# Kernel tuning notes

Measured on AMD Instinct MI355X. Metric: run time of the kernel, lower is better.

## Reference

```python
import jax, jax.numpy as jnp
import numpy as np


def _diag_perm(h, w):
    # Matches torch loop: offsets -(h-1)..w-1, within offset ordered by row i.
    ii, jj = np.meshgrid(np.arange(h), np.arange(w), indexing='ij')
    idx = np.lexsort((ii.ravel(), (jj - ii).ravel())).astype(np.int32)
    inv = np.argsort(idx).astype(np.int32)
    return jnp.asarray(idx), jnp.asarray(inv)


def _mamba(tok, ln_g, ln_b, Win, conv_w, conv_b, Wx, Wdt, bdt, A_log, Dp, Wout):
    # tok: (B, L, C). MambaLayer = LayerNorm + standard Mamba block.
    di, dc = conv_w.shape
    ds = A_log.shape[-1]
    dtr = Wdt.shape[-1]
    mu = tok.mean(-1, keepdims=True)
    var = ((tok - mu) ** 2).mean(-1, keepdims=True)
    t = (tok - mu) * jax.lax.rsqrt(var + 1e-5) * ln_g + ln_b
    xz = jnp.einsum('blc,ec->ble', t, Win)          # (B,L,2*di)
    xh, z = jnp.split(xz, 2, axis=-1)
    # causal depthwise conv over sequence
    xc = jnp.transpose(xh, (0, 2, 1))               # (B,di,L)
    xc = jax.lax.conv_general_dilated(
        xc, conv_w[:, None, :], (1,), [(dc - 1, 0)],
        dimension_numbers=('NCH', 'OIH', 'NCH'), feature_group_count=di)
    u = jax.nn.silu(jnp.transpose(xc, (0, 2, 1)) + conv_b)  # (B,L,di)
    proj = jnp.einsum('bld,ed->ble', u, Wx)
    dt_r, Bm, Cm = jnp.split(proj, [dtr, dtr + ds], axis=-1)
    dt = jax.nn.softplus(jnp.einsum('blr,dr->bld', dt_r, Wdt) + bdt)  # (B,L,di)
    A = -jnp.exp(A_log)                              # (di,ds)

    def step(h, inp):
        dt_t, B_t, C_t, u_t = inp                    # (B,di) (B,ds) (B,ds) (B,di)
        dA = jnp.exp(dt_t[..., None] * A)            # (B,di,ds)
        h = dA * h + dt_t[..., None] * B_t[:, None, :] * u_t[..., None]
        y = jnp.einsum('bds,bs->bd', h, C_t)
        return h, y

    h0 = jnp.zeros((u.shape[0], di, ds), u.dtype)
    _, ys = jax.lax.scan(step, h0, (jnp.moveaxis(dt, 1, 0), jnp.moveaxis(Bm, 1, 0),
                                    jnp.moveaxis(Cm, 1, 0), jnp.moveaxis(u, 1, 0)))
    y = jnp.moveaxis(ys, 0, 1) + u * Dp              # (B,L,di)
    y = y * jax.nn.silu(z)
    return jnp.einsum('bld,cd->blc', y, Wout)


def _forward(x, ln_g, ln_b, Win, conv_w, conv_b, Wx, Wdt, bdt, A_log, Dp, Wout):
    b, c, h, w = x.shape
    idx, inv = _diag_perm(h, w)

    def mam(d, tok):
        return _mamba(tok, ln_g[d], ln_b[d], Win[d], conv_w[d], conv_b[d],
                      Wx[d], Wdt[d], bdt[d], A_log[d], Dp[d], Wout[d])

    row_tok = x.reshape(b, c, h * w).transpose(0, 2, 1)
    row_feat = mam(0, row_tok).transpose(0, 2, 1).reshape(b, c, h, w)
    col_tok = x.transpose(0, 1, 3, 2).reshape(b, c, w * h).transpose(0, 2, 1)
    col_feat = mam(1, col_tok).transpose(0, 2, 1).reshape(b, c, w, h).transpose(0, 1, 3, 2)
    diag_feat = mam(2, row_tok[:, idx, :])[:, inv, :].transpose(0, 2, 1).reshape(b, c, h, w)
    xf = x[:, :, :, ::-1]
    anti_tok = xf.reshape(b, c, h * w).transpose(0, 2, 1)[:, idx, :]
    anti_feat = mam(3, anti_tok)[:, inv, :].transpose(0, 2, 1).reshape(b, c, h, w)[:, :, :, ::-1]
    gate = jax.nn.sigmoid((row_feat + col_feat + diag_feat + anti_feat) / 4.0)
    return x * gate


def setup_inputs() -> dict:
    key = jax.random.key(0)
    ks = jax.random.split(key, 8)
    B, C, H, W = 4, 96, 48, 48
    DI, DS, DC, DTR = 192, 16, 4, 6
    s = 0.05
    return {
        'x': jax.random.normal(ks[0], (B, C, H, W), jnp.float32),
        'ln_g': jnp.ones((4, C), jnp.float32),
        'ln_b': jnp.zeros((4, C), jnp.float32),
        'Win': jax.random.normal(ks[1], (4, 2 * DI, C), jnp.float32) * s,
        'conv_w': jax.random.normal(ks[2], (4, DI, DC), jnp.float32) * s,
        'conv_b': jnp.zeros((4, DI), jnp.float32),
        'Wx': jax.random.normal(ks[3], (4, DTR + 2 * DS, DI), jnp.float32) * s,
        'Wdt': jax.random.normal(ks[4], (4, DI, DTR), jnp.float32) * s,
        'bdt': jax.random.normal(ks[5], (4, DI), jnp.float32) * s,
        'A_log': jnp.log(jnp.broadcast_to(jnp.arange(1, DS + 1, dtype=jnp.float32), (4, DI, DS))),
        'Dp': jnp.ones((4, DI), jnp.float32),
        'Wout': jax.random.normal(ks[6], (4, C, DI), jnp.float32) * s,
    }


def reference(x, ln_g, ln_b, Win, conv_w, conv_b, Wx, Wdt, bdt, A_log, Dp, Wout):
    return _forward(x, ln_g, ln_b, Win, conv_w, conv_b, Wx, Wdt, bdt, A_log, Dp, Wout)
```

## Files before the change

kernel.cpp:

```cpp
#include <hip/hip_runtime.h>
#include <math.h>

#define LSEQ 2304
#define LC 32
#define NCH 72

typedef unsigned short u16;
typedef unsigned int u32;
typedef __attribute__((ext_vector_type(8))) short bf16x8;
typedef __attribute__((ext_vector_type(4))) float f32x4;

__device__ __forceinline__ float sigmoidf_(float v){ return 1.f/(1.f+__expf(-v)); }
__device__ __forceinline__ u16 f2b(float f){
  union{float f; u32 u;} v; v.f = f;
  u32 r = v.u + 0x7fffu + ((v.u >> 16) & 1u);
  return (u16)(r >> 16);
}
__device__ __forceinline__ float b2f(u16 h){
  union{u32 u; float f;} v; v.u = ((u32)h) << 16; return v.f;
}
__device__ __forceinline__ u16 f2h(float f){
  _Float16 h = (_Float16)f;
  union{_Float16 h; u16 u;} v; v.h = h; return v.u;
}
__device__ __forceinline__ float h2f(u16 u){
  union{u16 u; _Float16 h;} v; v.u = u; return (float)v.h;
}
__device__ __forceinline__ uint2 pack4(float a, float b, float c, float d){
  uint2 o;
  o.x = (u32)f2b(a) | ((u32)f2b(b) << 16);
  o.y = (u32)f2b(c) | ((u32)f2b(d) << 16);
  return o;
}
__device__ __forceinline__ float softplus_(float v){
  return fmaxf(v, 0.f) + __logf(1.f + __expf(-fabsf(v)));
}

__global__ void prep_fold(const float* __restrict__ Win, const float* __restrict__ ln_g,
                          const float* __restrict__ ln_b, const float* __restrict__ A_log,
                          const float* __restrict__ Wout, const float* __restrict__ Wx,
                          const float* __restrict__ Wdt, const float* __restrict__ bdt,
                          u16* __restrict__ WinMF, float* __restrict__ b2,
                          float* __restrict__ Aneg2, u16* __restrict__ WoutMF,
                          u16* __restrict__ Wcomb, float* __restrict__ bcomb,
                          int* __restrict__ g, int* __restrict__ flag){
  int i = blockIdx.x * 256 + threadIdx.x;
  if (i < LSEQ){
    int l = i;
    g[l] = l;
    g[LSEQ + l] = (l % 48) * 48 + l / 48;
    int p = i;
    int ii = p / 48, jj = p % 48, dd = jj - ii;
    int off = (dd <= 0) ? (47 + dd) * (48 + dd) / 2
                        : 1176 + 48 * (dd - 1) - dd * (dd - 1) / 2;
    int l2 = off + min(ii, jj);
    g[2 * LSEQ + l2] = p;
    g[3 * LSEQ + l2] = ii * 48 + 47 - jj;
  }
  if (i < 4*192*16){
    float a = -expf(A_log[i]);
    Aneg2[i] = a * 1.44269504f;
    int s = i & 15;
    float a0 = -expf(A_log[i - s]);
    if (fabsf(a - (float)(s + 1) * a0) > 1e-5f * fabsf(a) + 1e-30f)
      atomicOr(flag, 1);
  }
  if (i < 4*384*96){
    int d = i / 36864, r = i % 36864, c = r % 96;
    WinMF[i] = f2b(Win[i] * ln_g[d*96 + c]);
  }
  if (i < 4*96*192) WoutMF[i] = f2b(Wout[i]);
  if (i < 4*224*192){
    int d = i / 43008, r = i % 43008, e = r / 192, c = r % 192;
    float w;
    if (e < 192){
      const float* wdt = &Wdt[(size_t)(d*192 + e) * 6];
      w = 0.f;
      #pragma unroll
      for (int r6 = 0; r6 < 6; ++r6) w += wdt[r6] * Wx[(size_t)(d*38 + r6) * 192 + c];
    } else if (e < 208){
      w = Wx[(size_t)(d*38 + 6 + (e - 192)) * 192 + c];
    } else {
      w = Wx[(size_t)(d*38 + 22 + (e - 208)) * 192 + c];
    }
    Wcomb[i] = f2b(w);
  }
  if (i < 4*224){
    int d = i / 224, e = i % 224;
    bcomb[i] = (e < 192) ? bdt[d*192 + e] : 0.f;
  }
  if (i < 4*384){
    int d = i / 384;
    const float* wr = &Win[(size_t)i * 96];
    const float* lb = &ln_b[d * 96];
    float s = 0.f;
    for (int c = 0; c < 96; ++c) s += wr[c] * lb[c];
    b2[i] = s;
  }
}

__global__ __launch_bounds__(256) void ln_kernel(const float* __restrict__ x, u16* __restrict__ n){
  __shared__ float red[512];
  int tid = threadIdx.x;
  int s = tid & 63, q = tid >> 6;
  int T = blockIdx.x * 64 + s;
  int b = T / 2304, p = T % 2304;
  const float* xp = x + (size_t)b * 96 * 2304 + p;
  float vals[24];
  float sum = 0.f, ss = 0.f;
  #pragma unroll
  for (int k = 0; k < 24; ++k){
    float v = xp[(size_t)(q*24 + k) * 2304];
    vals[k] = v; sum += v; ss += v*v;
  }
  red[q*64 + s] = sum;
  red[256 + q*64 + s] = ss;
  __syncthreads();
  float S = red[s] + red[64+s] + red[128+s] + red[192+s];
  float Q = red[256+s] + red[320+s] + red[384+s] + red[448+s];
  float mu = S * (1.f/96.f);
  float var = Q * (1.f/96.f) - mu*mu;
  float rs = rsqrtf(var + 1e-5f);
  u32 w[12];
  #pragma unroll
  for (int k = 0; k < 12; ++k){
    float v0 = (vals[2*k]   - mu) * rs;
    float v1 = (vals[2*k+1] - mu) * rs;
    w[k] = (u32)f2b(v0) | ((u32)f2b(v1) << 16);
  }
  uint4* np_ = (uint4*)(n + (size_t)T * 96 + q*24);
  np_[0] = make_uint4(w[0], w[1], w[2],  w[3]);
  np_[1] = make_uint4(w[4], w[5], w[6],  w[7]);
  np_[2] = make_uint4(w[8], w[9], w[10], w[11]);
}

__global__ __launch_bounds__(256) void kproj(const u16* __restrict__ nbf,
    const u16* __restrict__ WinMF, const float* __restrict__ b2,
    u16* __restrict__ xz){
  int d = blockIdx.y;
  int wv = threadIdx.x >> 6, lane = threadIdx.x & 63;
  int lr = lane & 15, lg = lane >> 4;
  int r0 = blockIdx.x * 64 + wv * 16;
  const u16* Ap = nbf + (size_t)(r0 + lr) * 96 + lg * 8;
  bf16x8 tk0 = *(const bf16x8*)(Ap);
  bf16x8 tk1 = *(const bf16x8*)(Ap + 32);
  bf16x8 tk2 = *(const bf16x8*)(Ap + 64);
  const u16* Wb = WinMF + (size_t)d * 36864 + (size_t)lr * 96 + lg * 8;
  const float* b2d = b2 + d * 384;
  u16* out = xz + ((size_t)d * 9216 + r0 + lr) * 384;
  for (int grp = 0; grp < 3; ++grp){
    f32x4 acc[8];
    #pragma unroll
    for (int t = 0; t < 8; ++t)
      acc[t] = *(const f32x4*)&b2d[(grp*8 + t)*16 + lg*4];
    #pragma unroll
    for (int t = 0; t < 8; ++t){
      const u16* wp = Wb + (size_t)(grp*8 + t) * 1536;
      acc[t] = __builtin_amdgcn_mfma_f32_16x16x32_bf16(*(const bf16x8*)(wp     ), tk0, acc[t], 0, 0, 0);
      acc[t] = __builtin_amdgcn_mfma_f32_16x16x32_bf16(*(const bf16x8*)(wp + 32), tk1, acc[t], 0, 0, 0);
      acc[t] = __builtin_amdgcn_mfma_f32_16x16x32_bf16(*(const bf16x8*)(wp + 64), tk2, acc[t], 0, 0, 0);
    }
    #pragma unroll
    for (int t = 0; t < 8; ++t){
      uint2 o = pack4(acc[t][0], acc[t][1], acc[t][2], acc[t][3]);
      *(uint2*)&out[(grp*8 + t)*16 + lg*4] = o;
    }
  }
}

__global__ __launch_bounds__(256) void kconv(const u16* __restrict__ xz, const int* __restrict__ g,
    const float* __restrict__ conv_w, const float* __restrict__ conv_b,
    u16* __restrict__ u, u16* __restrict__ sz){
  __shared__ u16 xh[67][200];
  int d = blockIdx.z, b = blockIdx.y, l0 = blockIdx.x * 64;
  int tid = threadIdx.x;
  const int* gd = g + d * LSEQ;
  const u16* xzd = xz + (size_t)d * 9216 * 384 + (size_t)b * LSEQ * 384;
  for (int i = tid; i < 67*24; i += 256){
    int lt = i / 24, j = i % 24;
    int gl = l0 - 3 + lt;
    uint4 v = make_uint4(0u, 0u, 0u, 0u);
    if (gl >= 0){
      int p = gd[gl];
      v = *(const uint4*)(xzd + (size_t)p * 384 + j * 8);
    }
    *(uint4*)&xh[lt][j*8] = v;
  }
  size_t obase = ((size_t)(d*4 + b) * LSEQ + l0) * 192;
  for (int i = tid; i < 64*48; i += 256){
    int lt = i / 48, j = (i % 48) * 4;
    int p = gd[l0 + lt];
    uint2 zv = *(const uint2*)(xzd + (size_t)p * 384 + 192 + j);
    float z0 = b2f((u16)(zv.x & 0xffff)), z1 = b2f((u16)(zv.x >> 16));
    float z2 = b2f((u16)(zv.y & 0xffff)), z3 = b2f((u16)(zv.y >> 16));
    z0 *= sigmoidf_(z0); z1 *= sigmoidf_(z1); z2 *= sigmoidf_(z2); z3 *= sigmoidf_(z3);
    *(uint2*)(sz + obase + (size_t)lt * 192 + j) = pack4(z0, z1, z2, z3);
  }
  __syncthreads();
  for (int i = tid; i < 64*48; i += 256){
    int lt = i / 48, j = (i % 48) * 4;
    float a0 = conv_b[d*192 + j + 0];
    float a1 = conv_b[d*192 + j + 1];
    float a2 = conv_b[d*192 + j + 2];
    float a3 = conv_b[d*192 + j + 3];
    const float4 w0 = *(const float4*)&conv_w[(size_t)(d*192 + j + 0) * 4];
    const float4 w1 = *(const float4*)&conv_w[(size_t)(d*192 + j + 1) * 4];
    const float4 w2 = *(const float4*)&conv_w[(size_t)(d*192 + j + 2) * 4];
    const float4 w3 = *(const float4*)&conv_w[(size_t)(d*192 + j + 3) * 4];
    const float* w0p = (const float*)&w0;
    const float* w1p = (const float*)&w1;
    const float* w2p = (const float*)&w2;
    const float* w3p = (const float*)&w3;
    #pragma unroll
    for (int kk = 0; kk < 4; ++kk){
      uint2 xv = *(const uint2*)&xh[lt + kk][j];
      a0 += w0p[kk] * b2f((u16)(xv.x & 0xffff));
      a1 += w1p[kk] * b2f((u16)(xv.x >> 16));
      a2 += w2p[kk] * b2f((u16)(xv.y & 0xffff));
      a3 += w3p[kk] * b2f((u16)(xv.y >> 16));
    }
    a0 *= sigmoidf_(a0); a1 *= sigmoidf_(a1); a2 *= sigmoidf_(a2); a3 *= sigmoidf_(a3);
    *(uint2*)(u + obase + (size_t)lt * 192 + j) = pack4(a0, a1, a2, a3);
  }
}

__global__ __launch_bounds__(256) void kernBM(const u16* __restrict__ u,
    const u16* __restrict__ Wcomb, const float* __restrict__ bcomb,
    u16* __restrict__ dtb, float* __restrict__ Bm, float* __restrict__ Cm){
  __shared__ u16 ush[64 * 200];
  int d = blockIdx.y;
  int tid = threadIdx.x;
  int tile0 = blockIdx.x * 64;
  const u16* ub = u + ((size_t)d * 4 * LSEQ + tile0) * 192;
  for (int i = tid; i < 64*24; i += 256){
    int row = i / 24, c8 = i % 24;
    *(uint4*)&ush[row*200 + c8*8] = *(const uint4*)&ub[(size_t)row*192 + c8*8];
  }
  __syncthreads();
  int wv = tid >> 6, lane = tid & 63;
  int lr = lane & 15, lg = lane >> 4;
  const u16* urow = &ush[(wv*16 + lr)*200 + lg*8];
  bf16x8 tk[6];
  #pragma unroll
  for (int kc = 0; kc < 6; ++kc) tk[kc] = *(const bf16x8*)(urow + kc*32);
  const u16* Wb = Wcomb + (size_t)d * 224 * 192 + (size_t)lr * 192 + lg * 8;
  bf16x8 bw[2][6];
  #pragma unroll
  for (int kc = 0; kc < 6; ++kc) bw[0][kc] = *(const bf16x8*)(Wb + kc*32);
  size_t tokrow = (size_t)d * 4 * LSEQ + tile0 + wv*16 + lr;
  for (int t = 0; t < 14; ++t){
    int cur = t & 1;
    if (t < 13){
      const u16* wp = Wb + (size_t)(t + 1) * 3072;
      #pragma unroll
      for (int kc = 0; kc < 6; ++kc) bw[cur^1][kc] = *(const bf16x8*)(wp + kc*32);
    }
    f32x4 a = (f32x4){0.f, 0.f, 0.f, 0.f};
    #pragma unroll
    for (int kc = 0; kc < 6; ++kc)
      a = __builtin_amdgcn_mfma_f32_16x16x32_bf16(bw[cur][kc], tk[kc], a, 0, 0, 0);
    if (t < 12){
      f32x4 bb = *(const f32x4*)&bcomb[d*224 + t*16 + lg*4];
      float s0 = softplus_(a[0] + bb[0]);
      float s1 = softplus_(a[1] + bb[1]);
      float s2 = softplus_(a[2] + bb[2]);
      float s3 = softplus_(a[3] + bb[3]);
      uint2 o;
      o.x = (u32)f2h(s0) | ((u32)f2h(s1) << 16);
      o.y = (u32)f2h(s2) | ((u32)f2h(s3) << 16);
      *(uint2*)&dtb[tokrow * 192 + t*16 + lg*4] = o;
    } else if (t == 12){
      *(float4*)&Bm[tokrow * 16 + lg*4] = make_float4(a[0], a[1], a[2], a[3]);
    } else {
      *(float4*)&Cm[tokrow * 16 + lg*4] = make_float4(a[0], a[1], a[2], a[3]);
    }
  }
}

__global__ __launch_bounds__(192) void kernC1(const u16* __restrict__ dtb, const u16* __restrict__ u,
    const float* __restrict__ Bm, const float* __restrict__ Cm,
    const float* __restrict__ Aneg2, const int* __restrict__ flag,
    u16* __restrict__ hfin, float* __restrict__ Send, u32* __restrict__ yS){
  __shared__ float Bsh[LC*16];
  __shared__ float Csh[LC*16];
  __shared__ u16 dtsh[LC*192];
  __shared__ u16 ush2[LC*192];
  int ch = blockIdx.x, b = blockIdx.y, d = blockIdx.z;
  int seq = d*4 + b;
  int di = threadIdx.x;
  size_t tb = (size_t)seq * LSEQ + ch * LC;
  const float* bp = Bm + tb * 16;
  const float* cp = Cm + tb * 16;
  for (int i = di; i < LC*16; i += 192){ Bsh[i] = bp[i]; Csh[i] = cp[i]; }
  {
    const uint4* dt4 = (const uint4*)(dtb + tb * 192);
    const uint4* u4  = (const uint4*)(u   + tb * 192);
    #pragma unroll
    for (int i = di; i < 768; i += 192){
      *(uint4*)&dtsh[i*8] = dt4[i];
      *(uint4*)&ush2[i*8] = u4[i];
    }
  }
  u32* ySp = yS + tb * 192;
  float h[16];
  #pragma unroll
  for (int s = 0; s < 16; ++s) h[s] = 0.f;
  float Sacc = 0.f;
  __syncthreads();
  if (*flag == 0){
    float A2_0 = Aneg2[(d*192 + di) * 16];
    for (int j = 0; j < LC; ++j){
      float dtv = h2f(dtsh[j*192 + di]);
      float uv  = b2f(ush2[j*192 + di]);
      float Bs[16], Cs[16];
      {
        const float4* b4 = (const float4*)&Bsh[j * 16];
        const float4* c4 = (const float4*)&Csh[j * 16];
        #pragma unroll
        for (int q = 0; q < 4; ++q){
          float4 v = b4[q]; Bs[q*4]=v.x; Bs[q*4+1]=v.y; Bs[q*4+2]=v.z; Bs[q*4+3]=v.w;
          float4 w = c4[q]; Cs[q*4]=w.x; Cs[q*4+1]=w.y; Cs[q*4+2]=w.z; Cs[q*4+3]=w.w;
        }
      }
      float dtu = dtv * uv;
      float e1 = __builtin_amdgcn_exp2f(dtv * A2_0);
      float e2 = e1*e1, e4 = e2*e2, e8 = e4*e4;
      float p[8];
      p[0]=e1; p[1]=e2; p[2]=e1*e2; p[3]=e4; p[4]=e1*e4; p[5]=e2*e4; p[6]=p[2]*e4; p[7]=e8;
      float yv = 0.f;
      #pragma unroll
      for (int s = 0; s < 8; ++s){
        h[s] = p[s]*h[s] + dtu*Bs[s];
        yv += h[s]*Cs[s];
        float q = p[s]*e8;
        h[s+8] = q*h[s+8] + dtu*Bs[s+8];
        yv += h[s+8]*Cs[s+8];
      }
      Sacc += dtv;
      ySp[j*192 + di] = (u32)f2h(yv) | ((u32)f2h(Sacc) << 16);
    }
  } else {
    float A2[16];
    {
      const float4* ap = (const float4*)&Aneg2[(d*192 + di) * 16];
      #pragma unroll
      for (int q = 0; q < 4; ++q){ float4 a4 = ap[q]; A2[q*4]=a4.x; A2[q*4+1]=a4.y; A2[q*4+2]=a4.z; A2[q*4+3]=a4.w; }
    }
    for (int j = 0; j < LC; ++j){
      float dtv = h2f(dtsh[j*192 + di]);
      float uv  = b2f(ush2[j*192 + di]);
      float Bs[16], Cs[16];
      {
        const float4* b4 = (const float4*)&Bsh[j * 16];
        const float4* c4 = (const float4*)&Csh[j * 16];
        #pragma unroll
        for (int q = 0; q < 4; ++q){
          float4 v = b4[q]; Bs[q*4]=v.x; Bs[q*4+1]=v.y; Bs[q*4+2]=v.z; Bs[q*4+3]=v.w;
          float4 w = c4[q]; Cs[q*4]=w.x; Cs[q*4+1]=w.y; Cs[q*4+2]=w.z; Cs[q*4+3]=w.w;
        }
      }
      float dtu = dtv * uv;
      float yv = 0.f;
      #pragma unroll
      for (int s = 0; s < 16; ++s){
        h[s] = __builtin_amdgcn_exp2f(dtv * A2[s]) * h[s] + dtu * Bs[s];
        yv += h[s] * Cs[s];
      }
      Sacc += dtv;
      ySp[j*192 + di] = (u32)f2h(yv) | ((u32)f2h(Sacc) << 16);
    }
  }
  u16* hf = &hfin[((size_t)seq * NCH + ch) * 3072 + di * 16];
  uint4 o0, o1;
  o0.x = (u32)f2b(h[0])  | ((u32)f2b(h[1])  << 16);
  o0.y = (u32)f2b(h[2])  | ((u32)f2b(h[3])  << 16);
  o0.z = (u32)f2b(h[4])  | ((u32)f2b(h[5])  << 16);
  o0.w = (u32)f2b(h[6])  | ((u32)f2b(h[7])  << 16);
  o1.x = (u32)f2b(h[8])  | ((u32)f2b(h[9])  << 16);
  o1.y = (u32)f2b(h[10]) | ((u32)f2b(h[11]) << 16);
  o1.z = (u32)f2b(h[12]) | ((u32)f2b(h[13]) << 16);
  o1.w = (u32)f2b(h[14]) | ((u32)f2b(h[15]) << 16);
  *(uint4*)hf = o0;
  *(uint4*)(hf + 8) = o1;
  Send[((size_t)seq * NCH + ch) * 192 + di] = Sacc;
}

__global__ __launch_bounds__(256) void kernC2(const u16* __restrict__ hfin, const float* __restrict__ Send,
    const float* __restrict__ Aneg2, u16* __restrict__ hin){
  int t = blockIdx.x * 256 + threadIdx.x;
  int seq = t / 3072, q = t % 3072;
  int di = q >> 4, s = q & 15;
  int d = seq >> 2;
  float A2 = Aneg2[(d*192 + di)*16 + s];
  float hr = 0.f;
  const u16* hf = hfin + (size_t)seq * NCH * 3072 + q;
  u16* hi = hin + (size_t)seq * NCH * 3072 + q;
  const float* Se = Send + (size_t)seq * NCH * 192 + di;
  for (int ch = 0; ch < NCH; ch += 8){
    float Se8[8]; u16 hf8[8];
    #pragma unroll
    for (int k = 0; k < 8; ++k){
      Se8[k] = Se[(size_t)(ch+k) * 192];
      hf8[k] = hf[(size_t)(ch+k) * 3072];
    }
    #pragma unroll
    for (int k = 0; k < 8; ++k){
      hi[(size_t)(ch+k) * 3072] = f2b(hr);
      hr = b2f(hf8[k]) + __builtin_amdgcn_exp2f(A2 * Se8[k]) * hr;
    }
  }
}

__global__ __launch_bounds__(384) void kscan2out(const u32* __restrict__ yS, const u16* __restrict__ u,
    const float* __restrict__ Cm,
    const float* __restrict__ Aneg2, const int* __restrict__ flag, const u16* __restrict__ hin,
    const u16* __restrict__ sz, const float* __restrict__ Dp,
    const u16* __restrict__ WoutMF, const int* __restrict__ g,
    u16* __restrict__ feat){
  __shared__ float Csh[64*16];
  __shared__ u16 vsh[64][200];
  int b = blockIdx.y, d = blockIdx.z;
  int seq = d*4 + b;
  int l0 = blockIdx.x * 64;
  int tid = threadIdx.x;
  int gc = tid / 192, di = tid % 192;
  int ch = blockIdx.x * 2 + gc;
  {
    const float* cp = Cm + ((size_t)seq * LSEQ + l0) * 16;
    for (int i = tid; i < 64*16; i += 384) Csh[i] = cp[i];
  }
  float hs[16];
  {
    const uint4* hi4 = (const uint4*)&hin[((size_t)seq * NCH + ch) * 3072 + di * 16];
    uint4 v0 = hi4[0], v1 = hi4[1];
    hs[0]=b2f((u16)(v0.x&0xffff)); hs[1]=b2f((u16)(v0.x>>16));
    hs[2]=b2f((u16)(v0.y&0xffff)); hs[3]=b2f((u16)(v0.y>>16));
    hs[4]=b2f((u16)(v0.z&0xffff)); hs[5]=b2f((u16)(v0.z>>16));
    hs[6]=b2f((u16)(v0.w&0xffff)); hs[7]=b2f((u16)(v0.w>>16));
    hs[8]=b2f((u16)(v1.x&0xffff)); hs[9]=b2f((u16)(v1.x>>16));
    hs[10]=b2f((u16)(v1.y&0xffff)); hs[11]=b2f((u16)(v1.y>>16));
    hs[12]=b2f((u16)(v1.z&0xffff)); hs[13]=b2f((u16)(v1.z>>16));
    hs[14]=b2f((u16)(v1.w&0xffff)); hs[15]=b2f((u16)(v1.w>>16));
  }
  float Dpv = Dp[d*192 + di];
  size_t tb = (size_t)seq * LSEQ + ch * LC;
  const u32* ySp = yS + tb * 192;
  const u16* up  = u   + tb * 192;
  const u16* szp = sz  + tb * 192;
  __syncthreads();
  if (*flag == 0){
    float A2_0 = Aneg2[(d*192 + di) * 16];
    #pragma unroll
    for (int jb = 0; jb < 4; ++jb){
      u32 ys8[8]; u16 uu8[8], zz8[8];
      #pragma unroll
      for (int k = 0; k < 8; ++k){
        int j = jb*8 + k;
        ys8[k] = ySp[j*192 + di];
        uu8[k] = up[j*192 + di];
        zz8[k] = szp[j*192 + di];
      }
      #pragma unroll
      for (int k = 0; k < 8; ++k){
        int j = jb*8 + k;
        float yv = h2f((u16)(ys8[k] & 0xffff));
        float Sc = h2f((u16)(ys8[k] >> 16));
        float uv = b2f(uu8[k]);
        float Cs[16];
        {
          const float4* c4 = (const float4*)&Csh[(gc*32 + j) * 16];
          #pragma unroll
          for (int q = 0; q < 4; ++q){ float4 w = c4[q]; Cs[q*4]=w.x; Cs[q*4+1]=w.y; Cs[q*4+2]=w.z; Cs[q*4+3]=w.w; }
        }
        float e1 = __builtin_amdgcn_exp2f(Sc * A2_0);
        float e2 = e1*e1, e4 = e2*e2, e8 = e4*e4;
        float p[8];
        p[0]=e1; p[1]=e2; p[2]=e1*e2; p[3]=e4; p[4]=e1*e4; p[5]=e2*e4; p[6]=p[2]*e4; p[7]=e8;
        float corr = 0.f;
        #pragma unroll
        for (int s = 0; s < 8; ++s){
          corr += p[s]    * hs[s]   * Cs[s];
          corr += p[s]*e8 * hs[s+8] * Cs[s+8];
        }
        float szv = b2f(zz8[k]);
        vsh[gc*32 + j][di] = f2b((yv + corr + uv * Dpv) * szv);
      }
    }
  } else {
    float A2[16];
    {
      const float4* ap = (const float4*)&Aneg2[(d*192 + di) * 16];
      #pragma unroll
      for (int q = 0; q < 4; ++q){ float4 a4 = ap[q]; A2[q*4]=a4.x; A2[q*4+1]=a4.y; A2[q*4+2]=a4.z; A2[q*4+3]=a4.w; }
    }
    #pragma unroll
    for (int jb = 0; jb < 4; ++jb){
      u32 ys8[8]; u16 uu8[8], zz8[8];
      #pragma unroll
      for (int k = 0; k < 8; ++k){
        int j = jb*8 + k;
        ys8[k] = ySp[j*192 + di];
        uu8[k] = up[j*192 + di];
        zz8[k] = szp[j*192 + di];
      }
      #pragma unroll
      for (int k = 0; k < 8; ++k){
        int j = jb*8 + k;
        float yv = h2f((u16)(ys8[k] & 0xffff));
        float Sc = h2f((u16)(ys8[k] >> 16));
        float uv = b2f(uu8[k]);
        float Cs[16];
        {
          const float4* c4 = (const float4*)&Csh[(gc*32 + j) * 16];
          #pragma unroll
          for (int q = 0; q < 4; ++q){ float4 w = c4[q]; Cs[q*4]=w.x; Cs[q*4+1]=w.y; Cs[q*4+2]=w.z; Cs[q*4+3]=w.w; }
        }
        float corr = 0.f;
        #pragma unroll
        for (int s = 0; s < 16; ++s)
          corr += __builtin_amdgcn_exp2f(Sc * A2[s]) * hs[s] * Cs[s];
        float szv = b2f(zz8[k]);
        vsh[gc*32 + j][di] = f2b((yv + corr + uv * Dpv) * szv);
      }
    }
  }
  __syncthreads();
  if (tid < 256){
    int wv = tid >> 6, lane = tid & 63;
    int lr = lane & 15, lg = lane >> 4;
    bf16x8 tk[6];
    #pragma unroll
    for (int kc = 0; kc < 6; ++kc)
      tk[kc] = *(const bf16x8*)&vsh[wv*16 + lr][kc*32 + lg*8];
    const u16* Wb = WoutMF + (size_t)d * 18432 + (size_t)lr * 192 + lg * 8;
    f32x4 acc[6];
    #pragma unroll
    for (int t = 0; t < 6; ++t) acc[t] = (f32x4){0.f, 0.f, 0.f, 0.f};
    #pragma unroll
    for (int t = 0; t < 6; ++t){
      const u16* wp = Wb + (size_t)t * 3072;
      #pragma unroll
      for (int kc = 0; kc < 6; ++kc)
        acc[t] = __builtin_amdgcn_mfma_f32_16x16x32_bf16(*(const bf16x8*)(wp + kc*32), tk[kc], acc[t], 0, 0, 0);
    }
    u16* fd = feat + (size_t)seq * LSEQ * 96;
    int p = g[d*LSEQ + l0 + wv*16 + lr];
    #pragma unroll
    for (int t = 0; t < 6; ++t){
      uint2 o = pack4(acc[t][0], acc[t][1], acc[t][2], acc[t][3]);
      *(uint2*)&fd[(size_t)p * 96 + t*16 + lg*4] = o;
    }
  }
}

__global__ __launch_bounds__(256) void kernE(const float* __restrict__ x, const u16* __restrict__ feat,
    float* __restrict__ out){
  __shared__ float acc[64 * 97];
  int p0 = blockIdx.x * 64, b = blockIdx.y;
  int tid = threadIdx.x;
  const size_t DS_ = (size_t)4 * LSEQ * 96;
  size_t base = ((size_t)b * LSEQ + p0) * 96;
  for (int i = tid; i < 3072; i += 256){
    int pp = i / 48, c2 = (i % 48) * 2;
    size_t o = base + (size_t)pp * 96 + c2;
    u32 v0 = *(const u32*)(feat + o);
    u32 v1 = *(const u32*)(feat + DS_ + o);
    u32 v2 = *(const u32*)(feat + 2*DS_ + o);
    u32 v3 = *(const u32*)(feat + 3*DS_ + o);
    float s0 = b2f((u16)(v0 & 0xffff)) + b2f((u16)(v1 & 0xffff)) + b2f((u16)(v2 & 0xffff)) + b2f((u16)(v3 & 0xffff));
    float s1 = b2f((u16)(v0 >> 16)) + b2f((u16)(v1 >> 16)) + b2f((u16)(v2 >> 16)) + b2f((u16)(v3 >> 16));
    acc[pp*97 + c2] = s0;
    acc[pp*97 + c2 + 1] = s1;
  }
  __syncthreads();
  for (int i = tid; i < 6144; i += 256){
    int c = i / 64, pp = i % 64;
    size_t o = ((size_t)b * 96 + c) * LSEQ + p0 + pp;
    out[o] = x[o] * sigmoidf_(acc[pp*97 + c] * 0.25f);
  }
}

extern "C" void kernel_launch(void* const* d_in, const int* in_sizes, int n_in,
                              void* d_out, int out_size, void* d_ws, size_t ws_size,
                              hipStream_t stream) {
  const float* x      = (const float*)d_in[0];
  const float* ln_g   = (const float*)d_in[1];
  const float* ln_b   = (const float*)d_in[2];
  const float* Win    = (const float*)d_in[3];
  const float* conv_w = (const float*)d_in[4];
  const float* conv_b = (const float*)d_in[5];
  const float* Wx     = (const float*)d_in[6];
  const float* Wdt    = (const float*)d_in[7];
  const float* bdt    = (const float*)d_in[8];
  const float* A_log  = (const float*)d_in[9];
  const float* Dp     = (const float*)d_in[10];
  const float* Wout   = (const float*)d_in[11];

  char* W = (char*)d_ws;
  char* W0 = W;
  auto alloc = [&](size_t bytes) -> char* {
    char* p = W; W += (bytes + 255) & ~(size_t)255; return p;
  };
  int*   g      = (int*)  alloc((size_t)4 * LSEQ * 4);
  int*   flag   = (int*)  alloc(256);
  float* Aneg2  = (float*)alloc((size_t)4 * 192 * 16 * 4);
  float* b2     = (float*)alloc((size_t)4 * 384 * 4);
  u16*   WinMF  = (u16*)  alloc((size_t)4 * 384 * 96 * 2);
  u16*   WoutMF = (u16*)  alloc((size_t)4 * 96 * 192 * 2);
  u16*   Wcomb  = (u16*)  alloc((size_t)4 * 224 * 192 * 2);
  float* bcomb  = (float*)alloc((size_t)4 * 224 * 4);
  u16*   nbf    = (u16*)  alloc((size_t)9216 * 96 * 2);
  u16*   xz     = (u16*)  alloc((size_t)4 * 9216 * 384 * 2);
  u16*   ubf    = (u16*)  alloc((size_t)16 * LSEQ * 192 * 2);
  u16*   szbf   = (u16*)  alloc((size_t)16 * LSEQ * 192 * 2);
  u16*   dtb    = (u16*)  alloc((size_t)16 * LSEQ * 192 * 2);
  float* Bm     = (float*)alloc((size_t)16 * LSEQ * 16 * 4);
  float* Cm     = (float*)alloc((size_t)16 * LSEQ * 16 * 4);
  u32*   ySbuf  = (u32*)  alloc((size_t)16 * LSEQ * 192 * 4);
  float* Send   = (float*)alloc((size_t)16 * NCH * 192 * 4);
  u16*   hfin   = (u16*)  alloc((size_t)16 * NCH * 3072 * 2);
  u16*   hin    = (u16*)  alloc((size_t)16 * NCH * 3072 * 2);
  u16*   feat   = (u16*)  alloc((size_t)16 * LSEQ * 96 * 2);
  if ((size_t)(W - W0) > ws_size) return;

  hipMemsetAsync(flag, 0, sizeof(int), stream);
  prep_fold<<<768, 256, 0, stream>>>(Win, ln_g, ln_b, A_log, Wout, Wx, Wdt, bdt,
                                     WinMF, b2, Aneg2, WoutMF, Wcomb, bcomb, g, flag);
  ln_kernel<<<144, 256, 0, stream>>>(x, nbf);
  kproj<<<dim3(144, 4), 256, 0, stream>>>(nbf, WinMF, b2, xz);
  kconv<<<dim3(36, 4, 4), 256, 0, stream>>>(xz, g, conv_w, conv_b, ubf, szbf);
  kernBM<<<dim3(144, 4), 256, 0, stream>>>(ubf, Wcomb, bcomb, dtb, Bm, Cm);
  kernC1<<<dim3(NCH, 4, 4), 192, 0, stream>>>(dtb, ubf, Bm, Cm, Aneg2, flag, hfin, Send, ySbuf);
  kernC2<<<192, 256, 0, stream>>>(hfin, Send, Aneg2, hin);
  kscan2out<<<dim3(36, 4, 4), 384, 0, stream>>>(ySbuf, ubf, Cm, Aneg2, flag, hin, szbf, Dp,
                                                WoutMF, g, feat);
  kernE<<<dim3(36, 4), 256, 0, stream>>>(x, feat, (float*)d_out);
}
```

Measured before the change: 190.5 us.

## Fuse dt/B/C projection kernel into chunk-scan kernel via shared memory

Merges the MFMA projection that produces dt, B and C into the first chunked selective-scan kernel. Each 384-thread block projects a 64-token tile into shared memory and then runs two 32-token scan chunks from it. This removes the global dtb and Bm buffers and one kernel launch. The cost is that 128 threads sit idle during the projection phase, blocks are larger, more shared memory is used per block, and there are fewer blocks than the old scan grid.

```diff
diff --git a/kernel.cpp b/kernel.cpp
--- a/kernel.cpp
+++ b/kernel.cpp
@@ -224,98 +224,84 @@
   }
 }
 
-__global__ __launch_bounds__(256) void kernBM(const u16* __restrict__ u,
+__global__ __launch_bounds__(384) void kBMC1(const u16* __restrict__ u,
     const u16* __restrict__ Wcomb, const float* __restrict__ bcomb,
-    u16* __restrict__ dtb, float* __restrict__ Bm, float* __restrict__ Cm){
-  __shared__ u16 ush[64 * 200];
-  int d = blockIdx.y;
+    const float* __restrict__ Aneg2, const int* __restrict__ flag,
+    float* __restrict__ Cm, u32* __restrict__ yS,
+    u16* __restrict__ hfin, float* __restrict__ Send){
+  __shared__ u16 ush[64*200];
+  __shared__ u16 dtsh[64*200];
+  __shared__ float Bsh[64*20];
+  __shared__ float Csh[64*20];
+  int tile = blockIdx.x, b = blockIdx.y, d = blockIdx.z;
+  int seq = d*4 + b;
   int tid = threadIdx.x;
-  int tile0 = blockIdx.x * 64;
-  const u16* ub = u + ((size_t)d * 4 * LSEQ + tile0) * 192;
-  for (int i = tid; i < 64*24; i += 256){
+  size_t tokbase = (size_t)seq * LSEQ + tile * 64;
+  const u16* ub = u + tokbase * 192;
+  for (int i = tid; i < 64*24; i += 384){
     int row = i / 24, c8 = i % 24;
     *(uint4*)&ush[row*200 + c8*8] = *(const uint4*)&ub[(size_t)row*192 + c8*8];
   }
   __syncthreads();
-  int wv = tid >> 6, lane = tid & 63;
-  int lr = lane & 15, lg = lane >> 4;
-  const u16* urow = &ush[(wv*16 + lr)*200 + lg*8];
-  bf16x8 tk[6];
-  #pragma unroll
-  for (int kc = 0; kc < 6; ++kc) tk[kc] = *(const bf16x8*)(urow + kc*32);
-  const u16* Wb = Wcomb + (size_t)d * 224 * 192 + (size_t)lr * 192 + lg * 8;
-  bf16x8 bw[2][6];
-  #pragma unroll
-  for (int kc = 0; kc < 6; ++kc) bw[0][kc] = *(const bf16x8*)(Wb + kc*32);
-  size_t tokrow = (size_t)d * 4 * LSEQ + tile0 + wv*16 + lr;
-  for (int t = 0; t < 14; ++t){
-    int cur = t & 1;
-    if (t < 13){
-      const u16* wp = Wb + (size_t)(t + 1) * 3072;
-      #pragma unroll
-      for (int kc = 0; kc < 6; ++kc) bw[cur^1][kc] = *(const bf16x8*)(wp + kc*32);
-    }
-    f32x4 a = (f32x4){0.f, 0.f, 0.f, 0.f};
-    #pragma unroll
-    for (int kc = 0; kc < 6; ++kc)
-      a = __builtin_amdgcn_mfma_f32_16x16x32_bf16(bw[cur][kc], tk[kc], a, 0, 0, 0);
-    if (t < 12){
-      f32x4 bb = *(const f32x4*)&bcomb[d*224 + t*16 + lg*4];
-      float s0 = softplus_(a[0] + bb[0]);
-      float s1 = softplus_(a[1] + bb[1]);
-      float s2 = softplus_(a[2] + bb[2]);
-      float s3 = softplus_(a[3] + bb[3]);
-      uint2 o;
-      o.x = (u32)f2h(s0) | ((u32)f2h(s1) << 16);
-      o.y = (u32)f2h(s2) | ((u32)f2h(s3) << 16);
-      *(uint2*)&dtb[tokrow * 192 + t*16 + lg*4] = o;
-    } else if (t == 12){
-      *(float4*)&Bm[tokrow * 16 + lg*4] = make_float4(a[0], a[1], a[2], a[3]);
-    } else {
-      *(float4*)&Cm[tokrow * 16 + lg*4] = make_float4(a[0], a[1], a[2], a[3]);
-    }
-  }
-}
-
-__global__ __launch_bounds__(192) void kernC1(const u16* __restrict__ dtb, const u16* __restrict__ u,
-    const float* __restrict__ Bm, const float* __restrict__ Cm,
-    const float* __restrict__ Aneg2, const int* __restrict__ flag,
-    u16* __restrict__ hfin, float* __restrict__ Send, u32* __restrict__ yS){
-  __shared__ float Bsh[LC*16];
-  __shared__ float Csh[LC*16];
-  __shared__ u16 dtsh[LC*192];
-  __shared__ u16 ush2[LC*192];
-  int ch = blockIdx.x, b = blockIdx.y, d = blockIdx.z;
-  int seq = d*4 + b;
-  int di = threadIdx.x;
-  size_t tb = (size_t)seq * LSEQ + ch * LC;
-  const float* bp = Bm + tb * 16;
-  const float* cp = Cm + tb * 16;
-  for (int i = di; i < LC*16; i += 192){ Bsh[i] = bp[i]; Csh[i] = cp[i]; }
-  {
-    const uint4* dt4 = (const uint4*)(dtb + tb * 192);
-    const uint4* u4  = (const uint4*)(u   + tb * 192);
-    #pragma unroll
-    for (int i = di; i < 768; i += 192){
-      *(uint4*)&dtsh[i*8] = dt4[i];
-      *(uint4*)&ush2[i*8] = u4[i];
-    }
-  }
-  u32* ySp = yS + tb * 192;
+  if (tid < 256){
+    int wv = tid >> 6, lane = tid & 63;
+    int lr = lane & 15, lg = lane >> 4;
+    int row = wv*16 + lr;
+    const u16* urow = &ush[row*200 + lg*8];
+    bf16x8 tk[6];
+    #pragma unroll
+    for (int kc = 0; kc < 6; ++kc) tk[kc] = *(const bf16x8*)(urow + kc*32);
+    const u16* Wb = Wcomb + (size_t)d * 224 * 192 + (size_t)lr * 192 + lg * 8;
+    bf16x8 bw[2][6];
+    #pragma unroll
+    for (int kc = 0; kc < 6; ++kc) bw[0][kc] = *(const bf16x8*)(Wb + kc*32);
+    for (int t = 0; t < 14; ++t){
+      int cur = t & 1;
+      if (t < 13){
+        const u16* wp = Wb + (size_t)(t + 1) * 3072;
+        #pragma unroll
+        for (int kc = 0; kc < 6; ++kc) bw[cur^1][kc] = *(const bf16x8*)(wp + kc*32);
+      }
+      f32x4 a = (f32x4){0.f, 0.f, 0.f, 0.f};
+      #pragma unroll
+      for (int kc = 0; kc < 6; ++kc)
+        a = __builtin_amdgcn_mfma_f32_16x16x32_bf16(bw[cur][kc], tk[kc], a, 0, 0, 0);
+      if (t < 12){
+        f32x4 bb = *(const f32x4*)&bcomb[d*224 + t*16 + lg*4];
+        float s0 = softplus_(a[0] + bb[0]);
+        float s1 = softplus_(a[1] + bb[1]);
+        float s2 = softplus_(a[2] + bb[2]);
+        float s3 = softplus_(a[3] + bb[3]);
+        uint2 o;
+        o.x = (u32)f2h(s0) | ((u32)f2h(s1) << 16);
+        o.y = (u32)f2h(s2) | ((u32)f2h(s3) << 16);
+        *(uint2*)&dtsh[row*200 + t*16 + lg*4] = o;
+      } else if (t == 12){
+        *(float4*)&Bsh[row*20 + lg*4] = make_float4(a[0], a[1], a[2], a[3]);
+      } else {
+        *(float4*)&Csh[row*20 + lg*4] = make_float4(a[0], a[1], a[2], a[3]);
+        *(float4*)&Cm[(tokbase + row) * 16 + lg*4] = make_float4(a[0], a[1], a[2], a[3]);
+      }
+    }
+  }
+  __syncthreads();
+  int gc = tid / 192, di = tid % 192;
+  int ch = tile*2 + gc;
+  int j0 = gc*32;
+  u32* ySp = yS + (tokbase + j0) * 192;
   float h[16];
   #pragma unroll
   for (int s = 0; s < 16; ++s) h[s] = 0.f;
   float Sacc = 0.f;
-  __syncthreads();
   if (*flag == 0){
     float A2_0 = Aneg2[(d*192 + di) * 16];
     for (int j = 0; j < LC; ++j){
-      float dtv = h2f(dtsh[j*192 + di]);
-      float uv  = b2f(ush2[j*192 + di]);
+      float dtv = h2f(dtsh[(j0+j)*200 + di]);
+      float uv  = b2f(ush[(j0+j)*200 + di]);
       float Bs[16], Cs[16];
       {
-        const float4* b4 = (const float4*)&Bsh[j * 16];
-        const float4* c4 = (const float4*)&Csh[j * 16];
+        const float4* b4 = (const float4*)&Bsh[(j0+j)*20];
+        const float4* c4 = (const float4*)&Csh[(j0+j)*20];
         #pragma unroll
         for (int q = 0; q < 4; ++q){
           float4 v = b4[q]; Bs[q*4]=v.x; Bs[q*4+1]=v.y; Bs[q*4+2]=v.z; Bs[q*4+3]=v.w;
@@ -347,12 +333,12 @@
       for (int q = 0; q < 4; ++q){ float4 a4 = ap[q]; A2[q*4]=a4.x; A2[q*4+1]=a4.y; A2[q*4+2]=a4.z; A2[q*4+3]=a4.w; }
     }
     for (int j = 0; j < LC; ++j){
-      float dtv = h2f(dtsh[j*192 + di]);
-      float uv  = b2f(ush2[j*192 + di]);
+      float dtv = h2f(dtsh[(j0+j)*200 + di]);
+      float uv  = b2f(ush[(j0+j)*200 + di]);
       float Bs[16], Cs[16];
       {
-        const float4* b4 = (const float4*)&Bsh[j * 16];
-        const float4* c4 = (const float4*)&Csh[j * 16];
+        const float4* b4 = (const float4*)&Bsh[(j0+j)*20];
+        const float4* c4 = (const float4*)&Csh[(j0+j)*20];
         #pragma unroll
         for (int q = 0; q < 4; ++q){
           float4 v = b4[q]; Bs[q*4]=v.x; Bs[q*4+1]=v.y; Bs[q*4+2]=v.z; Bs[q*4+3]=v.w;
@@ -613,8 +599,6 @@
   u16*   xz     = (u16*)  alloc((size_t)4 * 9216 * 384 * 2);
   u16*   ubf    = (u16*)  alloc((size_t)16 * LSEQ * 192 * 2);
   u16*   szbf   = (u16*)  alloc((size_t)16 * LSEQ * 192 * 2);
-  u16*   dtb    = (u16*)  alloc((size_t)16 * LSEQ * 192 * 2);
-  float* Bm     = (float*)alloc((size_t)16 * LSEQ * 16 * 4);
   float* Cm     = (float*)alloc((size_t)16 * LSEQ * 16 * 4);
   u32*   ySbuf  = (u32*)  alloc((size_t)16 * LSEQ * 192 * 4);
   float* Send   = (float*)alloc((size_t)16 * NCH * 192 * 4);
@@ -629,8 +613,8 @@
   ln_kernel<<<144, 256, 0, stream>>>(x, nbf);
   kproj<<<dim3(144, 4), 256, 0, stream>>>(nbf, WinMF, b2, xz);
   kconv<<<dim3(36, 4, 4), 256, 0, stream>>>(xz, g, conv_w, conv_b, ubf, szbf);
-  kernBM<<<dim3(144, 4), 256, 0, stream>>>(ubf, Wcomb, bcomb, dtb, Bm, Cm);
-  kernC1<<<dim3(NCH, 4, 4), 192, 0, stream>>>(dtb, ubf, Bm, Cm, Aneg2, flag, hfin, Send, ySbuf);
+  kBMC1<<<dim3(36, 4, 4), 384, 0, stream>>>(ubf, Wcomb, bcomb, Aneg2, flag,
+                                            Cm, ySbuf, hfin, Send);
   kernC2<<<192, 256, 0, stream>>>(hfin, Send, Aneg2, hin);
   kscan2out<<<dim3(36, 4, 4), 384, 0, stream>>>(ySbuf, ubf, Cm, Aneg2, flag, hin, szbf, Dp,
                                                 WoutMF, g, feat);
```

Measured after the change: 190.5 us. About the same (+0.0%).
